# Performance work log

Hardware: AMD Instinct MI355X
Metric: run time of the kernel (lower is better)

Reference implementation:

```python
import jax, jax.numpy as jnp
import numpy as np

H = 4  # n_heads in nn.MultiheadAttention
LN_EPS = 1e-5


def _mha_seq1(x_q, x_kv, in_w, in_b, out_w, out_b):
    """torch nn.MultiheadAttention with batch_first and seq_len=1 on q and kv.
    x_q, x_kv: [B, F]. in_w: [3F, F] (packed q/k/v), out_w: [F, F].
    With a single kv position, softmax over the kv axis is identically 1,
    so the output equals out_proj(v); we still compute scores/softmax so the
    math (and zero grads to Wq/Wk) matches torch exactly.
    """
    B, F = x_q.shape
    dh = F // H
    wq, wk, wv = jnp.split(in_w, 3, axis=0)
    bq, bk, bv = jnp.split(in_b, 3, axis=0)
    q = (x_q @ wq.T + bq).reshape(B, H, dh)
    k = (x_kv @ wk.T + bk).reshape(B, H, dh)
    v = (x_kv @ wv.T + bv).reshape(B, H, dh)
    s = jnp.einsum('bhd,bhd->bh', q, k) / jnp.sqrt(jnp.asarray(dh, x_q.dtype))
    w = jax.nn.softmax(s[..., None], axis=-1)  # [B, H, 1] == 1
    o = (w * v).reshape(B, F)
    return o @ out_w.T + out_b


def _layer_norm(x, g, b):
    mu = jnp.mean(x, axis=-1, keepdims=True)
    var = jnp.mean(jnp.square(x - mu), axis=-1, keepdims=True)
    return (x - mu) * jax.lax.rsqrt(var + LN_EPS) * g + b


def setup_inputs() -> dict:
    key = jax.random.key(0)
    B, GD, TD, F = 16384, 1024, 1024, 2048
    ks = jax.random.split(key, 20)
    s = 0.02  # weight init scale
    return {
        'graph_feat': jax.random.normal(ks[0], (B, GD), jnp.float32),
        'temporal_feat': jax.random.normal(ks[1], (B, TD), jnp.float32),
        'gp_w': jax.random.normal(ks[2], (F, GD), jnp.float32) * s,
        'gp_b': jax.random.normal(ks[3], (F,), jnp.float32) * s,
        'tp_w': jax.random.normal(ks[4], (F, TD), jnp.float32) * s,
        'tp_b': jax.random.normal(ks[5], (F,), jnp.float32) * s,
        'in1_w': jax.random.normal(ks[6], (3 * F, F), jnp.float32) * s,
        'in1_b': jax.random.normal(ks[7], (3 * F,), jnp.float32) * s,
        'out1_w': jax.random.normal(ks[8], (F, F), jnp.float32) * s,
        'out1_b': jax.random.normal(ks[9], (F,), jnp.float32) * s,
        'in2_w': jax.random.normal(ks[10], (3 * F, F), jnp.float32) * s,
        'in2_b': jax.random.normal(ks[11], (3 * F,), jnp.float32) * s,
        'out2_w': jax.random.normal(ks[12], (F, F), jnp.float32) * s,
        'out2_b': jax.random.normal(ks[13], (F,), jnp.float32) * s,
        'gate_w': jax.random.normal(ks[14], (F, 2 * F), jnp.float32) * s,
        'gate_b': jax.random.normal(ks[15], (F,), jnp.float32) * s,
        'ln_g': jnp.ones((F,), jnp.float32),
        'ln_b': jnp.zeros((F,), jnp.float32),
        'lin_w': jax.random.normal(ks[16], (F, F), jnp.float32) * s,
        'lin_b': jax.random.normal(ks[17], (F,), jnp.float32) * s,
    }


def reference(graph_feat, temporal_feat, gp_w, gp_b, tp_w, tp_b,
              in1_w, in1_b, out1_w, out1_b, in2_w, in2_b, out2_w, out2_b,
              gate_w, gate_b, ln_g, ln_b, lin_w, lin_b):
    g = graph_feat @ gp_w.T + gp_b          # [B, F]
    t = temporal_feat @ tp_w.T + tp_b       # [B, F]
    attn1 = _mha_seq1(g, t, in1_w, in1_b, out1_w, out1_b)  # cross1(g, t, t)
    attn2 = _mha_seq1(t, g, in2_w, in2_b, out2_w, out2_b)  # cross2(t, g, g)
    cross = attn1 + attn2
    gate = jax.nn.sigmoid(jnp.concatenate([g, cross], axis=-1) @ gate_w.T + gate_b)
    fused = gate * g + (1.0 - gate) * cross
    fused = _layer_norm(fused + g, ln_g, ln_b)
    return fused @ lin_w.T + lin_b
```

## Files before the change

kernel.cpp:

```cpp
#include <hip/hip_runtime.h>
#include <stdint.h>

typedef __attribute__((ext_vector_type(8))) short short8;
typedef __attribute__((ext_vector_type(4))) float f32x4;

__device__ __forceinline__ unsigned short f2bf(float f) {
  union { float f; uint32_t u; } v; v.f = f;
  uint32_t u = v.u;
  u += 0x7FFF + ((u >> 16) & 1);
  return (unsigned short)(u >> 16);
}
__device__ __forceinline__ float bf2f(unsigned short h) {
  union { uint32_t u; float f; } v; v.u = ((uint32_t)h) << 16;
  return v.f;
}

__global__ void convcat2_kernel(const float* __restrict__ t,
                                const float* __restrict__ g,
                                unsigned short* __restrict__ out, long half) {
  long i = ((long)blockIdx.x * blockDim.x + threadIdx.x) * 8;
  const float* src;
  int colbase;
  if (i < half) { src = t; colbase = 0; }
  else { i -= half; src = g; colbase = 1024; }
  float4 a = *(const float4*)(src + i);
  float4 b = *(const float4*)(src + i + 4);
  short8 s;
  s[0] = (short)f2bf(a.x); s[1] = (short)f2bf(a.y);
  s[2] = (short)f2bf(a.z); s[3] = (short)f2bf(a.w);
  s[4] = (short)f2bf(b.x); s[5] = (short)f2bf(b.y);
  s[6] = (short)f2bf(b.z); s[7] = (short)f2bf(b.w);
  long row = i >> 10, col = i & 1023;
  *(short8*)(out + row * 2048 + colbase + col) = s;
}

__global__ void multiconv_kernel(const float* __restrict__ s0, unsigned short* d0, long n0,
                                 const float* __restrict__ s1, unsigned short* d1, long n1,
                                 const float* __restrict__ s2, unsigned short* d2, long n2,
                                 const float* __restrict__ s3, unsigned short* d3, long n3) {
  long i = ((long)blockIdx.x * blockDim.x + threadIdx.x) * 8;
  const float* s; unsigned short* d;
  if (i < n0) { s = s0; d = d0; }
  else if ((i -= n0) < n1) { s = s1; d = d1; }
  else if ((i -= n1) < n2) { s = s2; d = d2; }
  else { i -= n2; s = s3; d = d3; }
  float4 a = *(const float4*)(s + i);
  float4 b = *(const float4*)(s + i + 4);
  short8 o;
  o[0] = (short)f2bf(a.x); o[1] = (short)f2bf(a.y);
  o[2] = (short)f2bf(a.z); o[3] = (short)f2bf(a.w);
  o[4] = (short)f2bf(b.x); o[5] = (short)f2bf(b.y);
  o[6] = (short)f2bf(b.z); o[7] = (short)f2bf(b.w);
  *(short8*)(d + i) = o;
}

__global__ void convs_kernel(const float* __restrict__ in,
                             const float* __restrict__ scale,
                             unsigned short* __restrict__ out, int n) {
  long i = ((long)blockIdx.x * blockDim.x + threadIdx.x) * 8;
  if (i >= n) return;
  short8 s;
#pragma unroll
  for (int j = 0; j < 8; ++j)
    s[j] = (short)f2bf(in[i + j] * scale[(i + j) & 2047]);
  *(short8*)(out + i) = s;
}

__global__ void tconv2_kernel(const float* __restrict__ inA,
                              unsigned short* __restrict__ outA,
                              const float* __restrict__ inB,
                              unsigned short* __restrict__ outB, int R, int C) {
  const float* in = blockIdx.z ? inB : inA;
  unsigned short* out = blockIdx.z ? outB : outA;
  __shared__ float tile[32][33];
  int c0 = blockIdx.x * 32, r0 = blockIdx.y * 32;
  int tx = threadIdx.x, ty = threadIdx.y;
#pragma unroll
  for (int i = 0; i < 32; i += 8)
    tile[ty + i][tx] = in[(long)(r0 + ty + i) * C + c0 + tx];
  __syncthreads();
#pragma unroll
  for (int i = 0; i < 32; i += 8)
    out[(long)(c0 + ty + i) * R + r0 + tx] = f2bf(tile[tx][ty + i]);
}

enum { CE_PLAIN = 0, CE_WT = 1, CE_ACC = 2 };

template <int CE>
__global__ __launch_bounds__(256)
void compose_kernel(const unsigned short* __restrict__ A, int lda,
                    const unsigned short* __restrict__ W, int ldw,
                    unsigned short* C, int ldc,
                    unsigned short* Ct, long ctoff,
                    int K, int nmt,
                    int pairBase, long aoff, long woff, long coff,
                    int seg2Base, const unsigned short* A2, int lda2,
                    const unsigned short* W2, unsigned short* C2p) {
  constexpr int BK = 32;
  __shared__ unsigned short sA[128 * BK];
  __shared__ unsigned short sB[128 * BK];
  const int tid  = threadIdx.x;
  const int lane = tid & 63;
  const int wave = tid >> 6;
  const int wr = (wave >> 1) * 64;
  const int wc = (wave & 1) * 64;

  int bid = blockIdx.x;
  if (bid >= seg2Base) {
    bid -= seg2Base;
    A = A2; lda = lda2; W = W2; C = C2p;
  } else if (bid >= pairBase) {
    bid -= pairBase;
    A += aoff; W += woff; C += coff; Ct += ctoff;
  }
  const long tileM = (long)(bid % nmt) * 128;
  const long tileN = (long)(bid / nmt) * 128;

  const unsigned short* gA = A + (tileM + (tid >> 2)) * (long)lda + (tid & 3) * 8;
  const unsigned short* gB = W + (tileN + (tid >> 2)) * (long)ldw + (tid & 3) * 8;
  unsigned short* lA = sA + wave * 512;
  unsigned short* lB = sB + wave * 512;

  f32x4 acc[4][4] = {};
  const int fr = lane & 15;
  const int kb = (lane >> 4) * 8;

  for (int k0 = 0; k0 < K; k0 += BK) {
    __builtin_amdgcn_global_load_lds(
        (const __attribute__((address_space(1))) void*)(gA + k0),
        (__attribute__((address_space(3))) void*)(lA), 16, 0, 0);
    __builtin_amdgcn_global_load_lds(
        (const __attribute__((address_space(1))) void*)(gA + k0 + 64 * (long)lda),
        (__attribute__((address_space(3))) void*)(lA + 2048), 16, 0, 0);
    __builtin_amdgcn_global_load_lds(
        (const __attribute__((address_space(1))) void*)(gB + k0),
        (__attribute__((address_space(3))) void*)(lB), 16, 0, 0);
    __builtin_amdgcn_global_load_lds(
        (const __attribute__((address_space(1))) void*)(gB + k0 + 64 * (long)ldw),
        (__attribute__((address_space(3))) void*)(lB + 2048), 16, 0, 0);
    __syncthreads();

    short8 aF[4], bF[4];
#pragma unroll
    for (int m = 0; m < 4; ++m)
      aF[m] = *(const short8*)&sA[(wr + m * 16 + fr) * BK + kb];
#pragma unroll
    for (int n = 0; n < 4; ++n)
      bF[n] = *(const short8*)&sB[(wc + n * 16 + fr) * BK + kb];
#pragma unroll
    for (int m = 0; m < 4; ++m)
#pragma unroll
      for (int n = 0; n < 4; ++n)
        acc[m][n] = __builtin_amdgcn_mfma_f32_16x16x32_bf16(aF[m], bF[n], acc[m][n], 0, 0, 0);
    __syncthreads();
  }

  const int cr = (lane >> 4) * 4;
  const int cc = lane & 15;
#pragma unroll
  for (int m = 0; m < 4; ++m) {
    long r0 = tileM + wr + m * 16 + cr;
#pragma unroll
    for (int n = 0; n < 4; ++n) {
      long c = tileN + wc + n * 16 + cc;
#pragma unroll
      for (int r = 0; r < 4; ++r) {
        long idx = (r0 + r) * (long)ldc + c;
        float v = acc[m][n][r];
        if constexpr (CE == CE_ACC) v += bf2f(C[idx]);
        unsigned short bv = f2bf(v);
        C[idx] = bv;
        if constexpr (CE == CE_WT) Ct[c * 2048 + (r0 + r)] = bv;
      }
    }
  }
}

enum { EPI_BIAS = 0, EPI_LNF32 = 4 };

#define VMW(N) asm volatile("s_waitcnt vmcnt(" #N ")" ::: "memory")
#define SBAR() __builtin_amdgcn_s_barrier()

#define STG(D, OP, HALF, PTR, LD8)                                            \
  { char* lp_ = (char*)smem + ((D)*65536 + (OP)*32768 + (HALF)*16384 + w*2048); \
    __builtin_amdgcn_global_load_lds(                                         \
        (const __attribute__((address_space(1))) void*)(PTR),                 \
        (__attribute__((address_space(3))) void*)lp_, 16, 0, 0);              \
    __builtin_amdgcn_global_load_lds(                                         \
        (const __attribute__((address_space(1))) void*)((PTR) + (LD8)),       \
        (__attribute__((address_space(3))) void*)(lp_ + 1024), 16, 0, 0);     \
    (PTR) += 64; }
#define NOSTG ((void)0)

#define RDA(D, KK) ((KK) ? ((D) ? pA11 : pA01) : ((D) ? pA10 : pA00))
#define RDB(D, KK) ((KK) ? ((D) ? pB11 : pB01) : ((D) ? pB10 : pB00))

template <int EPI, int SWZ>
__global__ __launch_bounds__(512, 2)
void gemm8p_kernel(const unsigned short* __restrict__ A, int lda,
                   const unsigned short* __restrict__ W, int ldw,
                   int K, int ldc, int nmt,
                   const float* __restrict__ bias,
                   const float* __restrict__ bias2,
                   const float2* __restrict__ stats,
                   void* Cv) {
  __shared__ unsigned short smem[65536];

  const int tid = threadIdx.x, lane = tid & 63, w = tid >> 6;
  const int wm = w >> 2, wn = w & 3;

  int bid = blockIdx.x;
  int mt, nt;
  if (SWZ) {
    const int xcd = bid & 7, seq = bid >> 3;
    nt = seq >> 3;
    mt = xcd * 8 + (seq & 7);
  } else {
    mt = bid % nmt;
    nt = bid / nmt;
  }
  const long tileM = (long)mt * 256, tileN = (long)nt * 256;

  const int sRow = w * 16 + (lane >> 3);
  const int sCol = (((lane & 7) ^ ((lane >> 3) & 7)) * 8);
  const unsigned short* pSA0 = A + (tileM + sRow) * (long)lda + sCol;
  const unsigned short* pSA1 = pSA0 + 128 * (long)lda;
  const unsigned short* pSB0 = W + (tileN + sRow) * (long)ldw + sCol;
  const unsigned short* pSB1 = pSB0 + 128 * (long)ldw;
  const long lda8 = 8 * (long)lda, ldw8 = 8 * (long)ldw;

  const int fr = lane & 15, kc = lane >> 4, l7 = lane & 7;
  const char* pA00 = (const char*)smem + (wm * 16 + fr) * 128 + ((kc) ^ l7) * 16;
  const char* pA01 = (const char*)smem + (wm * 16 + fr) * 128 + ((4 + kc) ^ l7) * 16;
  const char* pA10 = pA00 + 65536;
  const char* pA11 = pA01 + 65536;
  const char* pB00 = (const char*)smem + 32768 + (wn * 16 + fr) * 128 + ((kc) ^ l7) * 16;
  const char* pB01 = (const char*)smem + 32768 + (wn * 16 + fr) * 128 + ((4 + kc) ^ l7) * 16;
  const char* pB10 = pB00 + 65536;
  const char* pB11 = pB01 + 65536;

  f32x4 acc[8][4] = {};
  short8 aH[4][2];
  short8 bqS[2][2][2];

#define MPHASE(D, MQ, LB, STGX)                                               \
  {                                                                           \
    _Pragma("unroll") for (int mi = 0; mi < 2; ++mi) {                        \
      aH[mi][0] = *(const short8*)(RDA(D, 0) + (MQ)*16384 + mi * 4096);       \
      aH[mi][1] = *(const short8*)(RDA(D, 1) + (MQ)*16384 + mi * 4096);       \
    }                                                                         \
    if (LB) {                                                                 \
      _Pragma("unroll") for (int q = 0; q < 2; ++q)                           \
      _Pragma("unroll") for (int ni = 0; ni < 2; ++ni) {                      \
        bqS[q][ni][0] = *(const short8*)(RDB(D, 0) + q * 16384 + ni * 8192);  \
        bqS[q][ni][1] = *(const short8*)(RDB(D, 1) + q * 16384 + ni * 8192);  \
      }                                                                       \
    }                                                                         \
    _Pragma("unroll") for (int mi = 2; mi < 4; ++mi) {                        \
      aH[mi][0] = *(const short8*)(RDA(D, 0) + (MQ)*16384 + mi * 4096);       \
      aH[mi][1] = *(const short8*)(RDA(D, 1) + (MQ)*16384 + mi * 4096);       \
    }                                                                         \
    STGX;                                                                     \
    __builtin_amdgcn_s_setprio(1);                                            \
    _Pragma("unroll") for (int mi = 0; mi < 4; ++mi)                          \
    _Pragma("unroll") for (int n = 0; n < 4; ++n) {                           \
      acc[(MQ)*4+mi][n] = __builtin_amdgcn_mfma_f32_16x16x32_bf16(            \
          aH[mi][0], bqS[n >> 1][n & 1][0], acc[(MQ)*4+mi][n], 0, 0, 0);      \
      acc[(MQ)*4+mi][n] = __builtin_amdgcn_mfma_f32_16x16x32_bf16(            \
          aH[mi][1], bqS[n >> 1][n & 1][1], acc[(MQ)*4+mi][n], 0, 0, 0);      \
    }                                                                         \
    __builtin_amdgcn_s_setprio(0);                                            \
  }

  STG(0, 0, 0, pSA0, lda8);
  STG(0, 1, 0, pSB0, ldw8);
  STG(0, 1, 1, pSB1, ldw8);
  STG(0, 0, 1, pSA1, lda8);
  STG(1, 0, 0, pSA0, lda8);
  STG(1, 1, 0, pSB0, ldw8);
  STG(1, 1, 1, pSB1, ldw8);
  VMW(8);
  SBAR();

  const int NIT = K / 128;
  for (int it = 0; it < NIT - 1; ++it) {
    MPHASE(0, 0, 1, STG(1, 0, 1, pSA1, lda8));            VMW(8); SBAR();
    MPHASE(0, 1, 0, STG(0, 0, 0, pSA0, lda8);
                    STG(0, 1, 0, pSB0, ldw8);
                    STG(0, 1, 1, pSB1, ldw8));            VMW(8); SBAR();
    MPHASE(1, 0, 1, STG(0, 0, 1, pSA1, lda8));            VMW(8); SBAR();
    MPHASE(1, 1, 0, STG(1, 0, 0, pSA0, lda8);
                    STG(1, 1, 0, pSB0, ldw8);
                    STG(1, 1, 1, pSB1, ldw8));            VMW(8); SBAR();
  }
  {
    MPHASE(0, 0, 1, STG(1, 0, 1, pSA1, lda8)); VMW(8); SBAR();
    MPHASE(0, 1, 0, NOSTG);                    VMW(2); SBAR();
    MPHASE(1, 0, 1, NOSTG);                    VMW(0); SBAR();
    MPHASE(1, 1, 0, NOSTG);
  }
#undef MPHASE

  const int cr = (lane >> 4) * 4;
  const int cc = lane & 15;
#pragma unroll
  for (int m = 0; m < 8; ++m) {
    long rr = tileM + (m >> 2) * 128 + (m & 3) * 32 + wm * 16 + cr;
#pragma unroll
    for (int n = 0; n < 4; ++n) {
      long c = tileN + (n >> 1) * 128 + (n & 1) * 64 + wn * 16 + cc;
      float b1 = bias ? bias[c] : 0.0f;
      float b2 = bias2 ? bias2[c] : 0.0f;
#pragma unroll
      for (int r = 0; r < 4; ++r) {
        long row = rr + r;
        long idx = row * (long)ldc + c;
        float v = acc[m][n][r];
        if constexpr (EPI == EPI_BIAS) {
          ((unsigned short*)Cv)[idx] = f2bf(v + b1 + b2);
        }
        if constexpr (EPI == EPI_LNF32) {
          float2 st = stats[row];
          ((float*)Cv)[idx] = v * st.y - st.y * st.x * b1 + b2;
        }
      }
    }
  }
}

__global__ __launch_bounds__(256) void fusestats_kernel(
    const unsigned short* __restrict__ CL, const unsigned short* __restrict__ G,
    unsigned short* __restrict__ PL, float2* __restrict__ stats) {
  const int row = blockIdx.x;
  const int t = threadIdx.x, lane = t & 63, wave = t >> 6;
  short8 xc = *(const short8*)&CL[(long)row * 4096 + t * 8];
  short8 xl = *(const short8*)&CL[(long)row * 4096 + 2048 + t * 8];
  short8 xg = *(const short8*)&G[(long)row * 2048 + t * 8];
  short8 o8;
  float s = 0.f, s2 = 0.f;
#pragma unroll
  for (int j = 0; j < 8; ++j) {
    float cv = bf2f((unsigned short)xc[j]);
    float lv = bf2f((unsigned short)xl[j]);
    float gv = bf2f((unsigned short)xg[j]);
    float gt = 1.0f / (1.0f + expf(-lv));
    unsigned short pb = f2bf(gt * gv + (1.0f - gt) * cv + gv);
    o8[j] = (short)pb;
    float x = bf2f(pb);
    s += x; s2 += x * x;
  }
  *(short8*)(PL + (long)row * 2048 + t * 8) = o8;
#pragma unroll
  for (int off = 1; off < 64; off <<= 1) {
    s  += __shfl_xor(s, off);
    s2 += __shfl_xor(s2, off);
  }
  __shared__ float red[8];
  if (lane == 0) { red[wave] = s; red[4 + wave] = s2; }
  __syncthreads();
  if (t == 0) {
    float ts  = red[0] + red[1] + red[2] + red[3];
    float ts2 = red[4] + red[5] + red[6] + red[7];
    float mean = ts * (1.0f / 2048.0f);
    float var  = ts2 * (1.0f / 2048.0f) - mean * mean;
    stats[row] = make_float2(mean, rsqrtf(var + 1e-5f));
  }
}

__device__ __forceinline__ float blkRed(float s, float* red, int lane, int wave) {
#pragma unroll
  for (int off = 1; off < 64; off <<= 1) s += __shfl_xor(s, off);
  if (lane == 0) red[wave] = s;
  __syncthreads();
  return red[0] + red[1] + red[2] + red[3];
}

__global__ __launch_bounds__(256) void biascompP_kernel(
    const unsigned short* __restrict__ wO1b, const unsigned short* __restrict__ wO2b,
    const unsigned short* __restrict__ Wc1, const unsigned short* __restrict__ Wc2,
    const float* __restrict__ bv1, const float* __restrict__ bv2,
    const float* __restrict__ tpb, const float* __restrict__ gpb,
    const float* __restrict__ o1b, const float* __restrict__ o2b,
    float* __restrict__ bcV) {
  __shared__ float red[4];
  int c = blockIdx.x, t = threadIdx.x, lane = t & 63, wave = t >> 6;
  int k = t * 8;
  float s = 0.f;
  short8 a1 = *(const short8*)(wO1b + (long)c * 2048 + k);
  short8 a2 = *(const short8*)(wO2b + (long)c * 2048 + k);
  short8 a3 = *(const short8*)(Wc1 + (long)c * 2048 + k);
  short8 a4 = *(const short8*)(Wc2 + (long)c * 2048 + k);
#pragma unroll
  for (int j = 0; j < 8; ++j)
    s += bf2f((unsigned short)a1[j]) * bv1[k + j]
       + bf2f((unsigned short)a2[j]) * bv2[k + j]
       + bf2f((unsigned short)a3[j]) * tpb[k + j]
       + bf2f((unsigned short)a4[j]) * gpb[k + j];
  float tot = blkRed(s, red, lane, wave);
  if (t == 0) bcV[c] = tot + o1b[c] + o2b[c];
}

__global__ __launch_bounds__(256) void bgateP_kernel(
    const float* __restrict__ gate_w, const float* __restrict__ gate_b,
    const float* __restrict__ gpb, const float* __restrict__ bcV,
    float* __restrict__ bgateV) {
  __shared__ float red[4];
  int n = blockIdx.x, t = threadIdx.x, lane = t & 63, wave = t >> 6;
  const float* row = gate_w + (long)n * 4096;
  float s = 0.f;
  int k = t * 8;
#pragma unroll
  for (int j = 0; j < 8; ++j)
    s += row[k + j] * gpb[k + j] + row[2048 + k + j] * bcV[k + j];
  float tot = blkRed(s, red, lane, wave);
  if (t == 0) bgateV[n] = tot + gate_b[n];
}

__global__ __launch_bounds__(256) void uvP_kernel(
    const unsigned short* __restrict__ wlinp, const float* __restrict__ lin_w,
    const float* __restrict__ ln_beta, const float* __restrict__ lin_b,
    float* __restrict__ uV, float* __restrict__ vV) {
  __shared__ float redu[4], redv[4];
  int n = blockIdx.x, t = threadIdx.x, lane = t & 63, wave = t >> 6;
  int k = t * 8;
  short8 a1 = *(const short8*)(wlinp + (long)n * 2048 + k);
  float u = 0.f, v = 0.f;
#pragma unroll
  for (int j = 0; j < 8; ++j) {
    u += bf2f((unsigned short)a1[j]);
    v += ln_beta[k + j] * lin_w[(long)n * 2048 + k + j];
  }
#pragma unroll
  for (int off = 1; off < 64; off <<= 1) {
    u += __shfl_xor(u, off);
    v += __shfl_xor(v, off);
  }
  if (lane == 0) { redu[wave] = u; redv[wave] = v; }
  __syncthreads();
  if (t == 0) {
    uV[n] = redu[0] + redu[1] + redu[2] + redu[3];
    vV[n] = redv[0] + redv[1] + redv[2] + redv[3] + lin_b[n];
  }
}

extern "C" void kernel_launch(void* const* d_in, const int* in_sizes, int n_in,
                              void* d_out, int out_size, void* d_ws, size_t ws_size,
                              hipStream_t stream) {
  const float* graph    = (const float*)d_in[0];
  const float* temporal = (const float*)d_in[1];
  const float* gp_w  = (const float*)d_in[2];
  const float* gp_b  = (const float*)d_in[3];
  const float* tp_w  = (const float*)d_in[4];
  const float* tp_b  = (const float*)d_in[5];
  const float* in1_w = (const float*)d_in[6];
  const float* in1_b = (const float*)d_in[7];
  const float* out1_w = (const float*)d_in[8];
  const float* out1_b = (const float*)d_in[9];
  const float* in2_w = (const float*)d_in[10];
  const float* in2_b = (const float*)d_in[11];
  const float* out2_w = (const float*)d_in[12];
  const float* out2_b = (const float*)d_in[13];
  const float* gate_w = (const float*)d_in[14];
  const float* gate_b = (const float*)d_in[15];
  const float* ln_g  = (const float*)d_in[16];
  const float* ln_b  = (const float*)d_in[17];
  const float* lin_w = (const float*)d_in[18];
  const float* lin_b = (const float*)d_in[19];

  const int Bm = 16384, F = 2048, GD = 1024;
  const long BF = (long)Bm * F, FF = (long)F * F, FG = (long)F * GD;

  unsigned short* TG   = (unsigned short*)d_ws;
  unsigned short* PL   = TG;
  unsigned short* Gbuf = TG + BF;
  unsigned short* wLIN = Gbuf + BF;
  unsigned short* wGP  = wLIN + FF;
  unsigned short* Wcg  = wGP + FG;
  unsigned short* Wcross = Wcg;
  unsigned short* Wgate  = Wcg + FF;
  float* bc2V   = (float*)(Wcg + 2 * FF);
  float* uV     = bc2V + 2 * F;
  float* vV     = uV + F;
  float2* stats = (float2*)(vV + F);

  unsigned short* DO      = (unsigned short*)d_out;
  unsigned short* wv1T    = DO;
  unsigned short* wv2T    = wv1T + FF;
  unsigned short* tpT     = wv2T + FF;
  unsigned short* gpT     = tpT + FG;
  unsigned short* Wc1     = gpT + FG;
  unsigned short* Wc2     = Wc1 + FF;
  unsigned short* wO1b    = Wc2 + FF;
  unsigned short* wO2b    = wO1b + FF;
  unsigned short* wGATEb  = wO2b + FF;
  unsigned short* WcrossT = wGATEb + 2 * FF;
  unsigned short* CL      = DO;

  hipMemsetAsync(Wgate, 0, FF * sizeof(unsigned short), stream);
  convcat2_kernel<<<dim3((unsigned)(2 * Bm * GD / 8 / 256)), 256, 0, stream>>>(
      temporal, graph, TG, (long)Bm * GD);
  {
    long ntot = FG + FF + FF + 2 * FF;
    multiconv_kernel<<<dim3((unsigned)(ntot / 8 / 256)), 256, 0, stream>>>(
        gp_w, wGP, FG, out1_w, wO1b, FF, out2_w, wO2b, FF, gate_w, wGATEb, 2 * FF);
  }
  convs_kernel<<<dim3((unsigned)(FF / 8 / 256)), 256, 0, stream>>>(lin_w, ln_g, wLIN, (int)FF);
  tconv2_kernel<<<dim3(F / 32, F / 32, 2), dim3(32, 8), 0, stream>>>(
      in1_w + 2 * FF, wv1T, in2_w + 2 * FF, wv2T, F, F);
  tconv2_kernel<<<dim3(GD / 32, F / 32, 2), dim3(32, 8), 0, stream>>>(
      tp_w, tpT, gp_w, gpT, F, GD);

  compose_kernel<CE_PLAIN><<<dim3(640), dim3(256), 0, stream>>>(
      wO1b, F, wv1T, F, Wc1, F, nullptr, 0, F, 16,
      256, wO2b - wO1b, wv2T - wv1T, Wc2 - Wc1,
      512, wGATEb, 2 * F, gpT, Wgate + GD);
  biascompP_kernel<<<dim3(F), dim3(256), 0, stream>>>(
      wO1b, wO2b, Wc1, Wc2, in1_b + 2 * F, in2_b + 2 * F, tp_b, gp_b,
      out1_b, out2_b, bc2V);
  compose_kernel<CE_WT><<<dim3(256), dim3(256), 0, stream>>>(
      Wc1, F, tpT, F, Wcross, F, WcrossT, (long)1024 * 2048, F, 16,
      128, Wc2 - Wc1, gpT - tpT, 1024,
      1 << 30, nullptr, 0, nullptr, nullptr);
  bgateP_kernel<<<dim3(F), dim3(256), 0, stream>>>(gate_w, gate_b, gp_b, bc2V,
                                                   bc2V + F);
  uvP_kernel<<<dim3(F), dim3(256), 0, stream>>>(wLIN, lin_w, ln_b, lin_b, uV, vV);
  compose_kernel<CE_ACC><<<dim3(256), dim3(256), 0, stream>>>(
      wGATEb + F, 2 * F, WcrossT, F, Wgate, F, nullptr, 0, F, 16,
      1 << 30, 0, 0, 0,
      1 << 30, nullptr, 0, nullptr, nullptr);

  dim3 blk(512);
  gemm8p_kernel<EPI_BIAS, 1><<<dim3(512), blk, 0, stream>>>(
      TG + GD, F, wGP, GD, GD, F, 0,
      gp_b, nullptr, nullptr, Gbuf);
  gemm8p_kernel<EPI_BIAS, 1><<<dim3(1024), blk, 0, stream>>>(
      TG, F, Wcg, F, F, 2 * F, 0,
      bc2V, nullptr, nullptr, CL);
  fusestats_kernel<<<dim3(Bm), dim3(256), 0, stream>>>(CL, Gbuf, PL, stats);
  gemm8p_kernel<EPI_LNF32, 1><<<dim3(512), blk, 0, stream>>>(
      PL, F, wLIN, F, F, F, 0,
      uV, vV, stats, (void*)d_out);
}
```

Before: 780.2 us.

## Fuse gate/cross epilogue and LayerNorm partial stats into the combined GEMM

The cross+gate GEMM now loads 128 rows of the cross weights and 128 matching rows of the gate weights into each 256-wide tile. Its epilogue then computes the sigmoid gate blend, writes the pre-LN bf16 activations directly, and emits per-tile row sum and sum-of-squares partials. A small reduce kernel turns these into LN stats, replacing the separate fusestats pass, which re-read a 2x-wide bf16 intermediate. The cost is a heavier GEMM epilogue: extra Gbuf reads, expf, shuffles and an LDS reduction with extra barriers.

Result: slower. 826.2 us (+5.9%).

```diff
diff --git a/kernel.cpp b/kernel.cpp
--- a/kernel.cpp
+++ b/kernel.cpp
@@ -176,7 +176,7 @@
   }
 }
 
-enum { EPI_BIAS = 0, EPI_LNF32 = 4 };
+enum { EPI_BIAS = 0, EPI_LNF32 = 4, EPI_FUSE = 5 };
 
 #define VMW(N) asm volatile("s_waitcnt vmcnt(" #N ")" ::: "memory")
 #define SBAR() __builtin_amdgcn_s_barrier()
@@ -198,10 +198,13 @@
 template <int EPI, int SWZ>
 __global__ __launch_bounds__(512, 2)
 void gemm8p_kernel(const unsigned short* __restrict__ A, int lda,
-                   const unsigned short* __restrict__ W, int ldw,
+                   const unsigned short* __restrict__ W,
+                   const unsigned short* __restrict__ W2b, int ldw,
                    int K, int ldc, int nmt,
                    const float* __restrict__ bias,
                    const float* __restrict__ bias2,
+                   const unsigned short* __restrict__ Gp,
+                   float2* __restrict__ partials,
                    const float2* __restrict__ stats,
                    void* Cv) {
   __shared__ unsigned short smem[65536];
@@ -225,8 +228,11 @@
   const int sCol = (((lane & 7) ^ ((lane >> 3) & 7)) * 8);
   const unsigned short* pSA0 = A + (tileM + sRow) * (long)lda + sCol;
   const unsigned short* pSA1 = pSA0 + 128 * (long)lda;
-  const unsigned short* pSB0 = W + (tileN + sRow) * (long)ldw + sCol;
-  const unsigned short* pSB1 = pSB0 + 128 * (long)ldw;
+  const long bRow = (EPI == EPI_FUSE) ? (long)nt * 128 : tileN;
+  const unsigned short* pSB0 = W + (bRow + sRow) * (long)ldw + sCol;
+  const unsigned short* pSB1 = (EPI == EPI_FUSE)
+      ? (W2b + (bRow + sRow) * (long)ldw + sCol)
+      : (pSB0 + 128 * (long)ldw);
   const long lda8 = 8 * (long)lda, ldw8 = 8 * (long)ldw;
 
   const int fr = lane & 15, kc = lane >> 4, l7 = lane & 7;
@@ -303,6 +309,51 @@
 
   const int cr = (lane >> 4) * 4;
   const int cc = lane & 15;
+
+  if constexpr (EPI == EPI_FUSE) {
+    SBAR();
+    float* sumP  = (float*)smem;
+    float* sumP2 = sumP + 1024;
+#pragma unroll
+    for (int m = 0; m < 8; ++m) {
+      const int rl0 = (m >> 2) * 128 + (m & 3) * 32 + wm * 16 + cr;
+#pragma unroll
+      for (int r = 0; r < 4; ++r) {
+        long row = tileM + rl0 + r;
+        float sA = 0.f, s2A = 0.f;
+#pragma unroll
+        for (int n = 0; n < 2; ++n) {
+          long col = (long)nt * 128 + n * 64 + wn * 16 + cc;
+          float cross = acc[m][n][r] + bias[col];
+          float logit = acc[m][n + 2][r] + bias2[col];
+          float gt = 1.0f / (1.0f + expf(-logit));
+          float gv = bf2f(Gp[row * 2048 + col]);
+          unsigned short pb = f2bf(gt * gv + (1.0f - gt) * cross + gv);
+          ((unsigned short*)Cv)[row * (long)ldc + col] = pb;
+          float x = bf2f(pb);
+          sA += x; s2A += x * x;
+        }
+#pragma unroll
+        for (int off = 1; off < 16; off <<= 1) {
+          sA  += __shfl_xor(sA, off);
+          s2A += __shfl_xor(s2A, off);
+        }
+        if ((lane & 15) == 0) {
+          int rl = rl0 + r;
+          sumP[rl * 4 + wn]  = sA;
+          sumP2[rl * 4 + wn] = s2A;
+        }
+      }
+    }
+    SBAR();
+    if (tid < 256) {
+      float s  = sumP[tid * 4] + sumP[tid * 4 + 1] + sumP[tid * 4 + 2] + sumP[tid * 4 + 3];
+      float s2 = sumP2[tid * 4] + sumP2[tid * 4 + 1] + sumP2[tid * 4 + 2] + sumP2[tid * 4 + 3];
+      partials[(tileM + tid) * 16 + nt] = make_float2(s, s2);
+    }
+    return;
+  }
+
 #pragma unroll
   for (int m = 0; m < 8; ++m) {
     long rr = tileM + (m >> 2) * 128 + (m & 3) * 32 + wm * 16 + cr;
@@ -328,43 +379,18 @@
   }
 }
 
-__global__ __launch_bounds__(256) void fusestats_kernel(
-    const unsigned short* __restrict__ CL, const unsigned short* __restrict__ G,
-    unsigned short* __restrict__ PL, float2* __restrict__ stats) {
-  const int row = blockIdx.x;
-  const int t = threadIdx.x, lane = t & 63, wave = t >> 6;
-  short8 xc = *(const short8*)&CL[(long)row * 4096 + t * 8];
-  short8 xl = *(const short8*)&CL[(long)row * 4096 + 2048 + t * 8];
-  short8 xg = *(const short8*)&G[(long)row * 2048 + t * 8];
-  short8 o8;
+__global__ __launch_bounds__(256) void lnreduce_kernel(
+    const float2* __restrict__ partials, float2* __restrict__ stats) {
+  int row = blockIdx.x * 256 + threadIdx.x;
   float s = 0.f, s2 = 0.f;
 #pragma unroll
-  for (int j = 0; j < 8; ++j) {
-    float cv = bf2f((unsigned short)xc[j]);
-    float lv = bf2f((unsigned short)xl[j]);
-    float gv = bf2f((unsigned short)xg[j]);
-    float gt = 1.0f / (1.0f + expf(-lv));
-    unsigned short pb = f2bf(gt * gv + (1.0f - gt) * cv + gv);
-    o8[j] = (short)pb;
-    float x = bf2f(pb);
-    s += x; s2 += x * x;
-  }
-  *(short8*)(PL + (long)row * 2048 + t * 8) = o8;
-#pragma unroll
-  for (int off = 1; off < 64; off <<= 1) {
-    s  += __shfl_xor(s, off);
-    s2 += __shfl_xor(s2, off);
-  }
-  __shared__ float red[8];
-  if (lane == 0) { red[wave] = s; red[4 + wave] = s2; }
-  __syncthreads();
-  if (t == 0) {
-    float ts  = red[0] + red[1] + red[2] + red[3];
-    float ts2 = red[4] + red[5] + red[6] + red[7];
-    float mean = ts * (1.0f / 2048.0f);
-    float var  = ts2 * (1.0f / 2048.0f) - mean * mean;
-    stats[row] = make_float2(mean, rsqrtf(var + 1e-5f));
-  }
+  for (int j = 0; j < 16; ++j) {
+    float2 p = partials[(long)row * 16 + j];
+    s += p.x; s2 += p.y;
+  }
+  float mean = s * (1.0f / 2048.0f);
+  float var  = s2 * (1.0f / 2048.0f) - mean * mean;
+  stats[row] = make_float2(mean, rsqrtf(var + 1e-5f));
 }
 
 __device__ __forceinline__ float blkRed(float s, float* red, int lane, int wave) {
@@ -471,7 +497,6 @@
   const long BF = (long)Bm * F, FF = (long)F * F, FG = (long)F * GD;
 
   unsigned short* TG   = (unsigned short*)d_ws;
-  unsigned short* PL   = TG;
   unsigned short* Gbuf = TG + BF;
   unsigned short* wLIN = Gbuf + BF;
   unsigned short* wGP  = wLIN + FF;
@@ -482,6 +507,8 @@
   float* uV     = bc2V + 2 * F;
   float* vV     = uV + F;
   float2* stats = (float2*)(vV + F);
+  float2* partials = stats + Bm;
+  unsigned short* PLn = (unsigned short*)(partials + (long)Bm * 16);
 
   unsigned short* DO      = (unsigned short*)d_out;
   unsigned short* wv1T    = DO;
@@ -494,7 +521,6 @@
   unsigned short* wO2b    = wO1b + FF;
   unsigned short* wGATEb  = wO2b + FF;
   unsigned short* WcrossT = wGATEb + 2 * FF;
-  unsigned short* CL      = DO;
 
   hipMemsetAsync(Wgate, 0, FF * sizeof(unsigned short), stream);
   convcat2_kernel<<<dim3((unsigned)(2 * Bm * GD / 8 / 256)), 256, 0, stream>>>(
@@ -531,13 +557,13 @@
 
   dim3 blk(512);
   gemm8p_kernel<EPI_BIAS, 1><<<dim3(512), blk, 0, stream>>>(
-      TG + GD, F, wGP, GD, GD, F, 0,
-      gp_b, nullptr, nullptr, Gbuf);
-  gemm8p_kernel<EPI_BIAS, 1><<<dim3(1024), blk, 0, stream>>>(
-      TG, F, Wcg, F, F, 2 * F, 0,
-      bc2V, nullptr, nullptr, CL);
-  fusestats_kernel<<<dim3(Bm), dim3(256), 0, stream>>>(CL, Gbuf, PL, stats);
+      TG + GD, F, wGP, nullptr, GD, GD, F, 0,
+      gp_b, nullptr, nullptr, nullptr, nullptr, Gbuf);
+  gemm8p_kernel<EPI_FUSE, 1><<<dim3(1024), blk, 0, stream>>>(
+      TG, F, Wcross, Wgate, F, F, F, 0,
+      bc2V, bc2V + F, Gbuf, partials, nullptr, PLn);
+  lnreduce_kernel<<<dim3(Bm / 256), dim3(256), 0, stream>>>(partials, stats);
   gemm8p_kernel<EPI_LNF32, 1><<<dim3(512), blk, 0, stream>>>(
-      PL, F, wLIN, F, F, F, 0,
-      uV, vV, stats, (void*)d_out);
-}
+      PLn, F, wLIN, nullptr, F, F, F, 0,
+      uV, vV, nullptr, nullptr, stats, (void*)d_out);
+}
```

## Reassociate weight composition to Wo·(Wv·Wp) and merge small prep kernels

Applied to the files above, without the earlier changes.

Reorders the weight-folding chain. Wv is first composed with the input projection into a 2048x1024 product, and that product is then multiplied by the output weight. This drops the full 2048x2048x2048 Wo·Wv products and the transpose-conversion of the in-proj V weights. The bias folding is restructured through a new q-vector kernel, the gate-bias and u/v reduction kernels are merged into one launch, and the six weight conversions are merged into one launch. It adds a scratch transpose output and changes rounding order, since intermediates are stored in bf16.

New measurement: 774.3 us. About the same (-0.7%).

```diff
diff --git a/kernel.cpp b/kernel.cpp
--- a/kernel.cpp
+++ b/kernel.cpp
@@ -34,16 +34,21 @@
   *(short8*)(out + row * 2048 + colbase + col) = s;
 }
 
-__global__ void multiconv_kernel(const float* __restrict__ s0, unsigned short* d0, long n0,
-                                 const float* __restrict__ s1, unsigned short* d1, long n1,
-                                 const float* __restrict__ s2, unsigned short* d2, long n2,
-                                 const float* __restrict__ s3, unsigned short* d3, long n3) {
+__global__ void multiconv6_kernel(
+    const float* __restrict__ s0, unsigned short* d0, long n0,
+    const float* __restrict__ s1, unsigned short* d1, long n1,
+    const float* __restrict__ s2, unsigned short* d2, long n2,
+    const float* __restrict__ s3, unsigned short* d3, long n3,
+    const float* __restrict__ s4, unsigned short* d4, long n4,
+    const float* __restrict__ s5, unsigned short* d5, long n5) {
   long i = ((long)blockIdx.x * blockDim.x + threadIdx.x) * 8;
   const float* s; unsigned short* d;
   if (i < n0) { s = s0; d = d0; }
   else if ((i -= n0) < n1) { s = s1; d = d1; }
   else if ((i -= n1) < n2) { s = s2; d = d2; }
-  else { i -= n2; s = s3; d = d3; }
+  else if ((i -= n2) < n3) { s = s3; d = d3; }
+  else if ((i -= n3) < n4) { s = s4; d = d4; }
+  else { i -= n4; s = s5; d = d5; }
   float4 a = *(const float4*)(s + i);
   float4 b = *(const float4*)(s + i + 4);
   short8 o;
@@ -95,7 +100,8 @@
                     int K, int nmt,
                     int pairBase, long aoff, long woff, long coff,
                     int seg2Base, const unsigned short* A2, int lda2,
-                    const unsigned short* W2, unsigned short* C2p) {
+                    const unsigned short* W2, unsigned short* C2p,
+                    unsigned short* C2t) {
   constexpr int BK = 32;
   __shared__ unsigned short sA[128 * BK];
   __shared__ unsigned short sB[128 * BK];
@@ -108,7 +114,7 @@
   int bid = blockIdx.x;
   if (bid >= seg2Base) {
     bid -= seg2Base;
-    A = A2; lda = lda2; W = W2; C = C2p;
+    A = A2; lda = lda2; W = W2; C = C2p; Ct = C2t;
   } else if (bid >= pairBase) {
     bid -= pairBase;
     A += aoff; W += woff; C += coff; Ct += ctoff;
@@ -375,11 +381,30 @@
   return red[0] + red[1] + red[2] + red[3];
 }
 
-__global__ __launch_bounds__(256) void biascompP_kernel(
+__global__ __launch_bounds__(256) void qvec_kernel(
+    const unsigned short* __restrict__ wv1, const unsigned short* __restrict__ wv2,
+    const float* __restrict__ tpb, const float* __restrict__ gpb,
+    float* __restrict__ qV) {
+  __shared__ float red[4];
+  int bid = blockIdx.x, t = threadIdx.x, lane = t & 63, wave = t >> 6;
+  const unsigned short* rowp;
+  const float* bvec;
+  if (bid < 2048) { rowp = wv1 + (long)bid * 2048; bvec = tpb; }
+  else { rowp = wv2 + (long)(bid - 2048) * 2048; bvec = gpb; }
+  int k = t * 8;
+  short8 a = *(const short8*)(rowp + k);
+  float s = 0.f;
+#pragma unroll
+  for (int j = 0; j < 8; ++j)
+    s += bf2f((unsigned short)a[j]) * bvec[k + j];
+  float tot = blkRed(s, red, lane, wave);
+  if (t == 0) qV[bid] = tot;
+}
+
+__global__ __launch_bounds__(256) void biascomp2_kernel(
     const unsigned short* __restrict__ wO1b, const unsigned short* __restrict__ wO2b,
-    const unsigned short* __restrict__ Wc1, const unsigned short* __restrict__ Wc2,
     const float* __restrict__ bv1, const float* __restrict__ bv2,
-    const float* __restrict__ tpb, const float* __restrict__ gpb,
+    const float* __restrict__ qV,
     const float* __restrict__ o1b, const float* __restrict__ o2b,
     float* __restrict__ bcV) {
   __shared__ float red[4];
@@ -388,58 +413,52 @@
   float s = 0.f;
   short8 a1 = *(const short8*)(wO1b + (long)c * 2048 + k);
   short8 a2 = *(const short8*)(wO2b + (long)c * 2048 + k);
-  short8 a3 = *(const short8*)(Wc1 + (long)c * 2048 + k);
-  short8 a4 = *(const short8*)(Wc2 + (long)c * 2048 + k);
 #pragma unroll
   for (int j = 0; j < 8; ++j)
-    s += bf2f((unsigned short)a1[j]) * bv1[k + j]
-       + bf2f((unsigned short)a2[j]) * bv2[k + j]
-       + bf2f((unsigned short)a3[j]) * tpb[k + j]
-       + bf2f((unsigned short)a4[j]) * gpb[k + j];
+    s += bf2f((unsigned short)a1[j]) * (bv1[k + j] + qV[k + j])
+       + bf2f((unsigned short)a2[j]) * (bv2[k + j] + qV[2048 + k + j]);
   float tot = blkRed(s, red, lane, wave);
   if (t == 0) bcV[c] = tot + o1b[c] + o2b[c];
 }
 
-__global__ __launch_bounds__(256) void bgateP_kernel(
+__global__ __launch_bounds__(256) void bgateuv_kernel(
     const float* __restrict__ gate_w, const float* __restrict__ gate_b,
     const float* __restrict__ gpb, const float* __restrict__ bcV,
-    float* __restrict__ bgateV) {
-  __shared__ float red[4];
-  int n = blockIdx.x, t = threadIdx.x, lane = t & 63, wave = t >> 6;
-  const float* row = gate_w + (long)n * 4096;
-  float s = 0.f;
-  int k = t * 8;
-#pragma unroll
-  for (int j = 0; j < 8; ++j)
-    s += row[k + j] * gpb[k + j] + row[2048 + k + j] * bcV[k + j];
-  float tot = blkRed(s, red, lane, wave);
-  if (t == 0) bgateV[n] = tot + gate_b[n];
-}
-
-__global__ __launch_bounds__(256) void uvP_kernel(
+    float* __restrict__ bgateV,
     const unsigned short* __restrict__ wlinp, const float* __restrict__ lin_w,
     const float* __restrict__ ln_beta, const float* __restrict__ lin_b,
     float* __restrict__ uV, float* __restrict__ vV) {
   __shared__ float redu[4], redv[4];
-  int n = blockIdx.x, t = threadIdx.x, lane = t & 63, wave = t >> 6;
+  int bid = blockIdx.x, t = threadIdx.x, lane = t & 63, wave = t >> 6;
   int k = t * 8;
-  short8 a1 = *(const short8*)(wlinp + (long)n * 2048 + k);
-  float u = 0.f, v = 0.f;
-#pragma unroll
-  for (int j = 0; j < 8; ++j) {
-    u += bf2f((unsigned short)a1[j]);
-    v += ln_beta[k + j] * lin_w[(long)n * 2048 + k + j];
-  }
-#pragma unroll
-  for (int off = 1; off < 64; off <<= 1) {
-    u += __shfl_xor(u, off);
-    v += __shfl_xor(v, off);
-  }
-  if (lane == 0) { redu[wave] = u; redv[wave] = v; }
-  __syncthreads();
-  if (t == 0) {
-    uV[n] = redu[0] + redu[1] + redu[2] + redu[3];
-    vV[n] = redv[0] + redv[1] + redv[2] + redv[3] + lin_b[n];
+  if (bid < 2048) {
+    const float* row = gate_w + (long)bid * 4096;
+    float s = 0.f;
+#pragma unroll
+    for (int j = 0; j < 8; ++j)
+      s += row[k + j] * gpb[k + j] + row[2048 + k + j] * bcV[k + j];
+    float tot = blkRed(s, redu, lane, wave);
+    if (t == 0) bgateV[bid] = tot + gate_b[bid];
+  } else {
+    int n = bid - 2048;
+    short8 a1 = *(const short8*)(wlinp + (long)n * 2048 + k);
+    float u = 0.f, v = 0.f;
+#pragma unroll
+    for (int j = 0; j < 8; ++j) {
+      u += bf2f((unsigned short)a1[j]);
+      v += ln_beta[k + j] * lin_w[(long)n * 2048 + k + j];
+    }
+#pragma unroll
+    for (int off = 1; off < 64; off <<= 1) {
+      u += __shfl_xor(u, off);
+      v += __shfl_xor(v, off);
+    }
+    if (lane == 0) { redu[wave] = u; redv[wave] = v; }
+    __syncthreads();
+    if (t == 0) {
+      uV[n] = redu[0] + redu[1] + redu[2] + redu[3];
+      vV[n] = redv[0] + redv[1] + redv[2] + redv[3] + lin_b[n];
+    }
   }
 }
 
@@ -481,53 +500,57 @@
   float* bc2V   = (float*)(Wcg + 2 * FF);
   float* uV     = bc2V + 2 * F;
   float* vV     = uV + F;
-  float2* stats = (float2*)(vV + F);
+  float* qV     = vV + F;
+  float2* stats = (float2*)(qV + 2 * F);
 
   unsigned short* DO      = (unsigned short*)d_out;
-  unsigned short* wv1T    = DO;
-  unsigned short* wv2T    = wv1T + FF;
-  unsigned short* tpT     = wv2T + FF;
+  unsigned short* wv1     = DO;
+  unsigned short* wv2     = wv1 + FF;
+  unsigned short* tpT     = wv2 + FF;
   unsigned short* gpT     = tpT + FG;
-  unsigned short* Wc1     = gpT + FG;
-  unsigned short* Wc2     = Wc1 + FF;
-  unsigned short* wO1b    = Wc2 + FF;
+  unsigned short* wO1b    = gpT + FG;
   unsigned short* wO2b    = wO1b + FF;
   unsigned short* wGATEb  = wO2b + FF;
-  unsigned short* WcrossT = wGATEb + 2 * FF;
+  unsigned short* P1      = wGATEb + 2 * FF;
+  unsigned short* P2      = P1 + FG;
+  unsigned short* P1T     = P2 + FG;
+  unsigned short* P2T     = P1T + FG;
+  unsigned short* WcrossT = P2T + FG;
+  unsigned short* Ctscr   = WcrossT + FF;
   unsigned short* CL      = DO;
 
   hipMemsetAsync(Wgate, 0, FF * sizeof(unsigned short), stream);
   convcat2_kernel<<<dim3((unsigned)(2 * Bm * GD / 8 / 256)), 256, 0, stream>>>(
       temporal, graph, TG, (long)Bm * GD);
   {
-    long ntot = FG + FF + FF + 2 * FF;
-    multiconv_kernel<<<dim3((unsigned)(ntot / 8 / 256)), 256, 0, stream>>>(
-        gp_w, wGP, FG, out1_w, wO1b, FF, out2_w, wO2b, FF, gate_w, wGATEb, 2 * FF);
+    long ntot = FG + 4 * FF + 2 * FF;
+    multiconv6_kernel<<<dim3((unsigned)(ntot / 8 / 256)), 256, 0, stream>>>(
+        gp_w, wGP, FG, out1_w, wO1b, FF, out2_w, wO2b, FF,
+        gate_w, wGATEb, 2 * FF,
+        in1_w + 2 * FF, wv1, FF, in2_w + 2 * FF, wv2, FF);
   }
   convs_kernel<<<dim3((unsigned)(FF / 8 / 256)), 256, 0, stream>>>(lin_w, ln_g, wLIN, (int)FF);
-  tconv2_kernel<<<dim3(F / 32, F / 32, 2), dim3(32, 8), 0, stream>>>(
-      in1_w + 2 * FF, wv1T, in2_w + 2 * FF, wv2T, F, F);
   tconv2_kernel<<<dim3(GD / 32, F / 32, 2), dim3(32, 8), 0, stream>>>(
       tp_w, tpT, gp_w, gpT, F, GD);
 
-  compose_kernel<CE_PLAIN><<<dim3(640), dim3(256), 0, stream>>>(
-      wO1b, F, wv1T, F, Wc1, F, nullptr, 0, F, 16,
-      256, wO2b - wO1b, wv2T - wv1T, Wc2 - Wc1,
-      512, wGATEb, 2 * F, gpT, Wgate + GD);
-  biascompP_kernel<<<dim3(F), dim3(256), 0, stream>>>(
-      wO1b, wO2b, Wc1, Wc2, in1_b + 2 * F, in2_b + 2 * F, tp_b, gp_b,
-      out1_b, out2_b, bc2V);
   compose_kernel<CE_WT><<<dim3(256), dim3(256), 0, stream>>>(
-      Wc1, F, tpT, F, Wcross, F, WcrossT, (long)1024 * 2048, F, 16,
-      128, Wc2 - Wc1, gpT - tpT, 1024,
-      1 << 30, nullptr, 0, nullptr, nullptr);
-  bgateP_kernel<<<dim3(F), dim3(256), 0, stream>>>(gate_w, gate_b, gp_b, bc2V,
-                                                   bc2V + F);
-  uvP_kernel<<<dim3(F), dim3(256), 0, stream>>>(wLIN, lin_w, ln_b, lin_b, uV, vV);
+      wv1, F, tpT, F, P1, GD, P1T, P2T - P1T, F, 16,
+      128, wv2 - wv1, gpT - tpT, P2 - P1,
+      1 << 30, nullptr, 0, nullptr, nullptr, nullptr);
+  qvec_kernel<<<dim3(2 * F), dim3(256), 0, stream>>>(wv1, wv2, tp_b, gp_b, qV);
+  compose_kernel<CE_WT><<<dim3(384), dim3(256), 0, stream>>>(
+      wO1b, F, P1T, F, Wcross, F, WcrossT, (long)1024 * 2048, F, 16,
+      128, wO2b - wO1b, P2T - P1T, 1024,
+      256, wGATEb, 2 * F, gpT, Wgate + GD, Ctscr);
+  biascomp2_kernel<<<dim3(F), dim3(256), 0, stream>>>(
+      wO1b, wO2b, in1_b + 2 * F, in2_b + 2 * F, qV, out1_b, out2_b, bc2V);
+  bgateuv_kernel<<<dim3(2 * F), dim3(256), 0, stream>>>(
+      gate_w, gate_b, gp_b, bc2V, bc2V + F,
+      wLIN, lin_w, ln_b, lin_b, uV, vV);
   compose_kernel<CE_ACC><<<dim3(256), dim3(256), 0, stream>>>(
       wGATEb + F, 2 * F, WcrossT, F, Wgate, F, nullptr, 0, F, 16,
       1 << 30, 0, 0, 0,
-      1 << 30, nullptr, 0, nullptr, nullptr);
+      1 << 30, nullptr, 0, nullptr, nullptr, nullptr);
 
   dim3 blk(512);
   gemm8p_kernel<EPI_BIAS, 1><<<dim3(512), blk, 0, stream>>>(
```
